# Optimization experiments

Measured on AMD Instinct MI355X. Metric: run time of the kernel, lower is better.

Reference implementation:

```python
import jax, jax.numpy as jnp
import numpy as np

B, S, D, H = 4, 2048, 512, 512

def setup_inputs() -> dict:
    key = jax.random.key(0)
    ks = jax.random.split(key, 9)
    sc_d = 1.0 / np.sqrt(D)
    sc_s = 1.0 / np.sqrt(S)
    return {
        "x": jax.random.normal(ks[0], (B, S, D), dtype=jnp.float32),
        "Wq": jax.random.normal(ks[1], (D, H), dtype=jnp.float32) * sc_d,
        "bq": jnp.zeros((H,), dtype=jnp.float32),
        "Wk": jax.random.normal(ks[2], (D, H), dtype=jnp.float32) * sc_d,
        "bk": jnp.zeros((H,), dtype=jnp.float32),
        "Wv": jax.random.normal(ks[3], (D, H), dtype=jnp.float32) * sc_d,
        "bv": jnp.zeros((H,), dtype=jnp.float32),
        "Wd": jax.random.normal(ks[4], (S, H), dtype=jnp.float32) * sc_s,
        "bd": jnp.zeros((H,), dtype=jnp.float32),
    }

def reference(x, Wq, bq, Wk, bk, Wv, bv, Wd, bd):
    # q, k, v: [B, S, H]
    q = x @ Wq + bq
    k = x @ Wk + bk
    v = x @ Wv + bv
    # raw scores: [B, S, S]
    qk = jnp.einsum('bsh,bth->bst', q, k)
    # Dense+sigmoid over the last (seqlen) axis: [B, S, H]
    dense_out = jax.nn.sigmoid(qk @ Wd + bd)
    # value weights: [B, S, S]
    vw = jnp.einsum('bsh,bth->bst', dense_out, v)
    # out: [B, S, D]
    return jnp.einsum('bst,btd->bsd', vw, x)
```

## Files before the change

kernel.cpp:

```cpp
#include <hip/hip_runtime.h>
#include <hip/hip_bf16.h>
#include <stdint.h>

#define BB 4
#define SS 2048
#define DD 512
#define HH 512

typedef __attribute__((ext_vector_type(8))) short short8;
typedef __attribute__((ext_vector_type(4))) float floatx4;

typedef __attribute__((address_space(3))) uint32_t lds_u32_t;
typedef const __attribute__((address_space(1))) uint32_t glb_u32_t;

__device__ __forceinline__ void gload_lds16(const void* g, void* l) {
  __builtin_amdgcn_global_load_lds((glb_u32_t*)g, (lds_u32_t*)l, 16, 0, 0);
}

__device__ __forceinline__ short f2bf(float f) {
  __hip_bfloat16 h = __float2bfloat16(f);
  return __builtin_bit_cast(short, h);
}

__device__ __forceinline__ float bf2f(short s) {
  uint32_t u = ((uint32_t)(uint16_t)s) << 16;
  return __builtin_bit_cast(float, u);
}

template <int BM>
__device__ __forceinline__ void gemm_mainloop(const short* __restrict__ Ab,
                                              const short* __restrict__ Bb,
                                              int lda, int ldb, int K,
                                              floatx4 (&acc)[BM / 32][4]) {
  constexpr int BK = 64;
  constexpr int MF = BM / 32;
  __shared__ short As[BM * BK];
  __shared__ short Bs[128 * BK];

  const int t = threadIdx.x;
  const int lane = t & 63;
  const int wid = t >> 6;
  const int wr = wid >> 1, wc = wid & 1;
  const int r16 = lane & 15;
  const int hi = lane >> 4;

  const int srow = t >> 3;
  const int schunk = t & 7;

#pragma unroll
  for (int i = 0; i < MF; i++)
#pragma unroll
    for (int j = 0; j < 4; j++) acc[i][j] = (floatx4)0.f;

  for (int k0 = 0; k0 < K; k0 += BK) {
#pragma unroll
    for (int s = 0; s < BM / 32; s++) {
      const int row = s * 32 + srow;
      const int g = schunk ^ (row & 7);
      gload_lds16(Ab + (long)row * lda + k0 + g * 8,
                  &As[row * BK + schunk * 8]);
    }
#pragma unroll
    for (int s = 0; s < 4; s++) {
      const int row = s * 32 + srow;
      const int g = schunk ^ (row & 7);
      gload_lds16(Bb + (long)row * ldb + k0 + g * 8,
                  &Bs[row * BK + schunk * 8]);
    }
    __syncthreads();

    short8 af[MF][2], bfr[4][2];
#pragma unroll
    for (int i = 0; i < MF; i++) {
      const int row = wr * (BM / 2) + i * 16 + r16;
      const int x7 = row & 7;
      af[i][0] = *(const short8*)&As[row * BK + (hi ^ x7) * 8];
      af[i][1] = *(const short8*)&As[row * BK + ((hi + 4) ^ x7) * 8];
    }
#pragma unroll
    for (int j = 0; j < 4; j++) {
      const int row = wc * 64 + j * 16 + r16;
      const int x7 = row & 7;
      bfr[j][0] = *(const short8*)&Bs[row * BK + (hi ^ x7) * 8];
      bfr[j][1] = *(const short8*)&Bs[row * BK + ((hi + 4) ^ x7) * 8];
    }
#pragma unroll
    for (int i = 0; i < MF; i++)
#pragma unroll
      for (int j = 0; j < 4; j++) {
        acc[i][j] = __builtin_amdgcn_mfma_f32_16x16x32_bf16(
            af[i][0], bfr[j][0], acc[i][j], 0, 0, 0);
        acc[i][j] = __builtin_amdgcn_mfma_f32_16x16x32_bf16(
            af[i][1], bfr[j][1], acc[i][j], 0, 0, 0);
      }
    __syncthreads();
  }
}

template <int BM, int EPI>
__device__ __forceinline__ void epilogue_std(floatx4 (&acc)[BM / 32][4],
                                             void* __restrict__ Cm, long c_base,
                                             const float* __restrict__ bias,
                                             int ldc, long row0, long col0) {
  const int lane = threadIdx.x & 63;
  const int wid = threadIdx.x >> 6;
  const int wr = wid >> 1, wc = wid & 1;
  const int r16 = lane & 15;
#pragma unroll
  for (int i = 0; i < BM / 32; i++) {
    const long rbase = row0 + wr * (BM / 2) + i * 16 + (lane >> 4) * 4;
#pragma unroll
    for (int j = 0; j < 4; j++) {
      const long col = col0 + wc * 64 + j * 16 + r16;
      float bv = 0.f;
      if (EPI == 2) bv = bias[col];
#pragma unroll
      for (int rg = 0; rg < 4; rg++) {
        float v = acc[i][j][rg];
        if (EPI == 2) v = 1.f / (1.f + __expf(-(v + bv)));
        const long idx = c_base + (rbase + rg) * ldc + col;
        if (EPI == 3)
          ((float*)Cm)[idx] = v;
        else
          ((__hip_bfloat16*)Cm)[idx] = __float2bfloat16(v);
      }
    }
  }
}

template <int BM, int EPI>
__global__ __launch_bounds__(256) void gemm_bt(
    const short* __restrict__ A, const short* __restrict__ Bm,
    void* __restrict__ Cm, const float* __restrict__ bias, int K, int lda,
    int ldb, int ldc, long sA, long sB, long sC) {
  const int bz = blockIdx.z;
  floatx4 acc[BM / 32][4];
  const long row0 = (long)blockIdx.x * BM, col0 = (long)blockIdx.y * 128;
  gemm_mainloop<BM>(A + bz * sA + row0 * lda, Bm + bz * sB + col0 * ldb, lda,
                    ldb, K, acc);
  epilogue_std<BM, EPI>(acc, Cm, bz * sC, bias, ldc, row0, col0);
}

__global__ __launch_bounds__(256) void gemm_qkv(
    const short* __restrict__ xb, const short* __restrict__ WT,
    const float* __restrict__ bcat, short* __restrict__ q,
    short* __restrict__ kT, short* __restrict__ vT) {
  floatx4 acc[4][4];
  const long row0 = (long)blockIdx.x * 128;
  const int y = blockIdx.y;
  gemm_mainloop<128>(xb + row0 * DD, WT + (long)y * 128 * DD, DD, DD, DD, acc);

  const int lane = threadIdx.x & 63;
  const int wid = threadIdx.x >> 6;
  const int wr = wid >> 1, wc = wid & 1;
  const int r16 = lane & 15;
  const int hi4 = (lane >> 4) * 4;
  const int mode = y >> 2;
  const int b = (int)(row0 >> 11);
  const int sblk = (int)(row0 & 2047);
  short* tp = (mode == 1) ? kT : vT;
#pragma unroll
  for (int i = 0; i < 4; i++) {
    const int s0 = sblk + wr * 64 + i * 16 + hi4;
#pragma unroll
    for (int j = 0; j < 4; j++) {
      const int colg = y * 128 + wc * 64 + j * 16 + r16;
      const float bv = bcat[colg];
      short o[4];
#pragma unroll
      for (int rg = 0; rg < 4; rg++) o[rg] = f2bf(acc[i][j][rg] + bv);
      if (mode == 0) {
#pragma unroll
        for (int rg = 0; rg < 4; rg++)
          q[((long)b * SS + s0 + rg) * HH + colg] = o[rg];
      } else {
        const int cl = colg - mode * 512;
        *(uint64_t*)&tp[((long)b * HH + cl) * SS + s0] = *(uint64_t*)o;
      }
    }
  }
}

__global__ __launch_bounds__(256) void gemm_dual_split(
    const short* __restrict__ WdT, const short* __restrict__ kT,
    short* __restrict__ partM2, const short* __restrict__ xT,
    const short* __restrict__ vT, short* __restrict__ partM3) {
  const int bz = blockIdx.z;
  const int tb = bz >> 2, sp = bz & 3;
  const int task = tb >> 2, b = tb & 3;
  const short* A = (task ? xT + (long)b * HH * SS : WdT) + sp * 512;
  const short* B = (task ? vT : kT) + (long)b * HH * SS + sp * 512;
  short* C = (task ? partM3 : partM2) + ((long)(tb & 3) * 4 + sp) * HH * HH;
  floatx4 acc[2][4];
  const long row0 = (long)blockIdx.x * 64, col0 = (long)blockIdx.y * 128;
  gemm_mainloop<64>(A + row0 * SS, B + col0 * SS, SS, SS, 512, acc);
  epilogue_std<64, 0>(acc, C, 0, nullptr, HH, row0, col0);
}

__global__ __launch_bounds__(256) void reduce_part(
    const short* __restrict__ partM2, const short* __restrict__ partM3,
    short* __restrict__ M2, short* __restrict__ M3t) {
  const int z = blockIdx.z;
  const int b = z & 3;
  const short* src = (z < 4 ? partM2 : partM3) + (long)b * 4 * HH * HH;
  short* dst = (z < 4 ? M2 : M3t) + (long)b * HH * HH;
  const long i = ((long)blockIdx.x * 256 + threadIdx.x) * 8;
  float s[8];
#pragma unroll
  for (int j = 0; j < 8; j++) s[j] = 0.f;
#pragma unroll
  for (int sp = 0; sp < 4; sp++) {
    short8 v = *(const short8*)&src[(long)sp * HH * HH + i];
#pragma unroll
    for (int j = 0; j < 8; j++) s[j] += bf2f(v[j]);
  }
  short o[8];
#pragma unroll
  for (int j = 0; j < 8; j++) o[j] = f2bf(s[j]);
  *(short8*)&dst[i] = *(short8*)o;
}

__global__ void prep(const float* __restrict__ x, const float* __restrict__ Wq,
                     const float* __restrict__ Wk, const float* __restrict__ Wv,
                     const float* __restrict__ Wd, const float* __restrict__ bq,
                     const float* __restrict__ bk, const float* __restrict__ bv,
                     short* __restrict__ xb, short* __restrict__ xT,
                     short* __restrict__ WT, short* __restrict__ WdT,
                     float* __restrict__ bcat) {
  __shared__ float tile[32][33];
  const int z = blockIdx.z, yb = blockIdx.y;
  const int tx = threadIdx.x, ty = threadIdx.y;
  if (z < 4) {
    const long b = z;
    const float* in = x + b * SS * DD;
    const int c0 = blockIdx.x * 32, r0 = yb * 32;
#pragma unroll
    for (int i = 0; i < 32; i += 8) {
      float v = in[(long)(r0 + ty + i) * DD + c0 + tx];
      tile[ty + i][tx] = v;
      xb[(b * SS + r0 + ty + i) * DD + c0 + tx] = f2bf(v);
    }
    __syncthreads();
#pragma unroll
    for (int i = 0; i < 32; i += 8)
      xT[(b * DD + c0 + ty + i) * SS + r0 + tx] = f2bf(tile[tx][ty + i]);
  } else if (z < 7) {
    const int w = z - 4;
    if (yb < 16) {
      const float* in = w == 0 ? Wq : (w == 1 ? Wk : Wv);
      short* out = WT + (long)w * HH * DD;
      const int c0 = blockIdx.x * 32, r0 = yb * 32;
#pragma unroll
      for (int i = 0; i < 32; i += 8)
        tile[ty + i][tx] = in[(long)(r0 + ty + i) * HH + c0 + tx];
      __syncthreads();
#pragma unroll
      for (int i = 0; i < 32; i += 8)
        out[(long)(c0 + ty + i) * DD + r0 + tx] = f2bf(tile[tx][ty + i]);
    } else if (w == 0 && yb < 22 && blockIdx.x == 0) {
      const int i = (yb - 16) * 256 + ty * 32 + tx;
      bcat[i] = i < 512 ? bq[i] : (i < 1024 ? bk[i - 512] : bv[i - 1024]);
    }
  } else {
    const int c0 = blockIdx.x * 32, r0 = yb * 32;
#pragma unroll
    for (int i = 0; i < 32; i += 8)
      tile[ty + i][tx] = Wd[(long)(r0 + ty + i) * HH + c0 + tx];
    __syncthreads();
#pragma unroll
    for (int i = 0; i < 32; i += 8)
      WdT[(long)(c0 + ty + i) * SS + r0 + tx] = f2bf(tile[tx][ty + i]);
  }
}

extern "C" void kernel_launch(void* const* d_in, const int* in_sizes, int n_in,
                              void* d_out, int out_size, void* d_ws,
                              size_t ws_size, hipStream_t stream) {
  (void)in_sizes;
  (void)n_in;
  (void)out_size;
  (void)ws_size;
  const float* x = (const float*)d_in[0];
  const float* Wq = (const float*)d_in[1];
  const float* bq = (const float*)d_in[2];
  const float* Wk = (const float*)d_in[3];
  const float* bk = (const float*)d_in[4];
  const float* Wv = (const float*)d_in[5];
  const float* bv = (const float*)d_in[6];
  const float* Wd = (const float*)d_in[7];
  const float* bd = (const float*)d_in[8];

  char* w = (char*)d_ws;
  auto alloc = [&](size_t bytes) {
    char* p = w;
    w += (bytes + 255) & ~(size_t)255;
    return p;
  };
  short* xb = (short*)alloc((size_t)BB * SS * DD * 2);
  short* xT = (short*)alloc((size_t)BB * DD * SS * 2);
  short* WT = (short*)alloc((size_t)3 * HH * DD * 2);
  short* WdT = (short*)alloc((size_t)HH * SS * 2);
  float* bcat = (float*)alloc((size_t)3 * HH * 4);
  short* q = (short*)alloc((size_t)BB * SS * HH * 2);
  short* kT = (short*)alloc((size_t)BB * HH * SS * 2);
  short* vT = (short*)alloc((size_t)BB * HH * SS * 2);
  short* partM2 = (short*)alloc((size_t)BB * 4 * HH * HH * 2);
  short* partM3 = (short*)alloc((size_t)BB * 4 * HH * HH * 2);
  short* M2 = (short*)alloc((size_t)BB * HH * HH * 2);
  short* M3t = (short*)alloc((size_t)BB * DD * HH * 2);
  short* dense = (short*)alloc((size_t)BB * SS * HH * 2);

  dim3 tb(32, 8);
  prep<<<dim3(16, 64, 8), tb, 0, stream>>>(x, Wq, Wk, Wv, Wd, bq, bk, bv, xb,
                                           xT, WT, WdT, bcat);

  gemm_qkv<<<dim3(BB * SS / 128, 12, 1), 256, 0, stream>>>(xb, WT, bcat, q, kT,
                                                           vT);
  gemm_dual_split<<<dim3(8, 4, 32), 256, 0, stream>>>(WdT, kT, partM2, xT, vT,
                                                      partM3);
  reduce_part<<<dim3(128, 1, 8), 256, 0, stream>>>(partM2, partM3, M2, M3t);
  gemm_bt<64, 2><<<dim3(SS / 64, HH / 128, BB), 256, 0, stream>>>(
      q, M2, dense, bd, HH, HH, HH, HH, (long)SS * HH, (long)HH * HH,
      (long)SS * HH);
  gemm_bt<64, 3><<<dim3(SS / 64, DD / 128, BB), 256, 0, stream>>>(
      dense, M3t, d_out, nullptr, HH, HH, HH, DD, (long)SS * HH, (long)DD * HH,
      (long)SS * DD);
}
```

Before: 81.87 us.

## Fuse dense-sigmoid GEMM and output GEMM into one kernel via LDS

```diff
diff --git a/kernel.cpp b/kernel.cpp
--- a/kernel.cpp
+++ b/kernel.cpp
@@ -97,11 +97,11 @@
   }
 }
 
-template <int BM, int EPI>
-__device__ __forceinline__ void epilogue_std(floatx4 (&acc)[BM / 32][4],
-                                             void* __restrict__ Cm, long c_base,
-                                             const float* __restrict__ bias,
-                                             int ldc, long row0, long col0) {
+template <int BM>
+__device__ __forceinline__ void epilogue_bf16(floatx4 (&acc)[BM / 32][4],
+                                              short* __restrict__ Cm,
+                                              long c_base, int ldc, long row0,
+                                              long col0) {
   const int lane = threadIdx.x & 63;
   const int wid = threadIdx.x >> 6;
   const int wr = wid >> 1, wc = wid & 1;
@@ -112,33 +112,11 @@
 #pragma unroll
     for (int j = 0; j < 4; j++) {
       const long col = col0 + wc * 64 + j * 16 + r16;
-      float bv = 0.f;
-      if (EPI == 2) bv = bias[col];
-#pragma unroll
-      for (int rg = 0; rg < 4; rg++) {
-        float v = acc[i][j][rg];
-        if (EPI == 2) v = 1.f / (1.f + __expf(-(v + bv)));
-        const long idx = c_base + (rbase + rg) * ldc + col;
-        if (EPI == 3)
-          ((float*)Cm)[idx] = v;
-        else
-          ((__hip_bfloat16*)Cm)[idx] = __float2bfloat16(v);
-      }
-    }
-  }
-}
-
-template <int BM, int EPI>
-__global__ __launch_bounds__(256) void gemm_bt(
-    const short* __restrict__ A, const short* __restrict__ Bm,
-    void* __restrict__ Cm, const float* __restrict__ bias, int K, int lda,
-    int ldb, int ldc, long sA, long sB, long sC) {
-  const int bz = blockIdx.z;
-  floatx4 acc[BM / 32][4];
-  const long row0 = (long)blockIdx.x * BM, col0 = (long)blockIdx.y * 128;
-  gemm_mainloop<BM>(A + bz * sA + row0 * lda, Bm + bz * sB + col0 * ldb, lda,
-                    ldb, K, acc);
-  epilogue_std<BM, EPI>(acc, Cm, bz * sC, bias, ldc, row0, col0);
+#pragma unroll
+      for (int rg = 0; rg < 4; rg++)
+        Cm[c_base + (rbase + rg) * ldc + col] = f2bf(acc[i][j][rg]);
+    }
+  }
 }
 
 __global__ __launch_bounds__(256) void gemm_qkv(
@@ -194,7 +172,7 @@
   floatx4 acc[2][4];
   const long row0 = (long)blockIdx.x * 64, col0 = (long)blockIdx.y * 128;
   gemm_mainloop<64>(A + row0 * SS, B + col0 * SS, SS, SS, 512, acc);
-  epilogue_std<64, 0>(acc, C, 0, nullptr, HH, row0, col0);
+  epilogue_bf16<64>(acc, C, 0, HH, row0, col0);
 }
 
 __global__ __launch_bounds__(256) void reduce_part(
@@ -218,6 +196,142 @@
 #pragma unroll
   for (int j = 0; j < 8; j++) o[j] = f2bf(s[j]);
   *(short8*)&dst[i] = *(short8*)o;
+}
+
+__global__ __launch_bounds__(512) void gemm_fused23(
+    const short* __restrict__ q, const short* __restrict__ M2,
+    const short* __restrict__ M3t, const float* __restrict__ bd,
+    float* __restrict__ out) {
+  __shared__ short As[32 * 64];
+  __shared__ short Bs[512 * 64];
+  __shared__ short Ds[32 * 512];
+
+  const int b = blockIdx.z;
+  const long row0 = (long)blockIdx.x * 32;
+  const short* qs = q + ((long)b * SS + row0) * HH;
+  const short* B1 = M2 + (long)b * HH * HH;
+  const short* B2 = M3t + (long)b * DD * HH;
+
+  const int t = threadIdx.x;
+  const int lane = t & 63;
+  const int w = t >> 6;
+  const int r16 = lane & 15;
+  const int hi = lane >> 4;
+
+  floatx4 acc[2][4];
+#pragma unroll
+  for (int i = 0; i < 2; i++)
+#pragma unroll
+    for (int j = 0; j < 4; j++) acc[i][j] = (floatx4)0.f;
+
+  for (int k0 = 0; k0 < 512; k0 += 64) {
+    if (t < 256) {
+      const int row = t >> 3, slot = t & 7;
+      const int g = slot ^ (row & 7);
+      gload_lds16(qs + (long)row * HH + k0 + g * 8, &As[row * 64 + slot * 8]);
+    }
+#pragma unroll
+    for (int i = 0; i < 8; i++) {
+      const int c = i * 512 + t;
+      const int row = c >> 3, slot = c & 7;
+      const int g = slot ^ (row & 7);
+      gload_lds16(B1 + (long)row * HH + k0 + g * 8, &Bs[row * 64 + slot * 8]);
+    }
+    __syncthreads();
+    short8 af[2][2], bf[4][2];
+#pragma unroll
+    for (int i = 0; i < 2; i++) {
+      const int row = i * 16 + r16;
+      const int x7 = row & 7;
+      af[i][0] = *(const short8*)&As[row * 64 + (hi ^ x7) * 8];
+      af[i][1] = *(const short8*)&As[row * 64 + ((hi + 4) ^ x7) * 8];
+    }
+#pragma unroll
+    for (int j = 0; j < 4; j++) {
+      const int row = w * 64 + j * 16 + r16;
+      const int x7 = row & 7;
+      bf[j][0] = *(const short8*)&Bs[row * 64 + (hi ^ x7) * 8];
+      bf[j][1] = *(const short8*)&Bs[row * 64 + ((hi + 4) ^ x7) * 8];
+    }
+#pragma unroll
+    for (int i = 0; i < 2; i++)
+#pragma unroll
+      for (int j = 0; j < 4; j++) {
+        acc[i][j] = __builtin_amdgcn_mfma_f32_16x16x32_bf16(af[i][0], bf[j][0],
+                                                            acc[i][j], 0, 0, 0);
+        acc[i][j] = __builtin_amdgcn_mfma_f32_16x16x32_bf16(af[i][1], bf[j][1],
+                                                            acc[i][j], 0, 0, 0);
+      }
+    __syncthreads();
+  }
+
+#pragma unroll
+  for (int i = 0; i < 2; i++)
+#pragma unroll
+    for (int j = 0; j < 4; j++) {
+      const int col = w * 64 + j * 16 + r16;
+      const float bv = bd[col];
+#pragma unroll
+      for (int rg = 0; rg < 4; rg++) {
+        const int row = i * 16 + hi * 4 + rg;
+        const float v = 1.f / (1.f + __expf(-(acc[i][j][rg] + bv)));
+        Ds[row * 512 + (((col >> 3) ^ (row & 7)) << 3) + (col & 7)] = f2bf(v);
+      }
+    }
+#pragma unroll
+  for (int i = 0; i < 2; i++)
+#pragma unroll
+    for (int j = 0; j < 4; j++) acc[i][j] = (floatx4)0.f;
+  __syncthreads();
+
+  for (int k0 = 0; k0 < 512; k0 += 64) {
+#pragma unroll
+    for (int i = 0; i < 8; i++) {
+      const int c = i * 512 + t;
+      const int row = c >> 3, slot = c & 7;
+      const int g = slot ^ (row & 7);
+      gload_lds16(B2 + (long)row * HH + k0 + g * 8, &Bs[row * 64 + slot * 8]);
+    }
+    __syncthreads();
+    short8 af[2][2], bf[4][2];
+    const int kc = k0 >> 3;
+#pragma unroll
+    for (int i = 0; i < 2; i++) {
+      const int row = i * 16 + r16;
+      const int x7 = row & 7;
+      af[i][0] = *(const short8*)&Ds[row * 512 + (kc + (hi ^ x7)) * 8];
+      af[i][1] = *(const short8*)&Ds[row * 512 + (kc + ((hi + 4) ^ x7)) * 8];
+    }
+#pragma unroll
+    for (int j = 0; j < 4; j++) {
+      const int row = w * 64 + j * 16 + r16;
+      const int x7 = row & 7;
+      bf[j][0] = *(const short8*)&Bs[row * 64 + (hi ^ x7) * 8];
+      bf[j][1] = *(const short8*)&Bs[row * 64 + ((hi + 4) ^ x7) * 8];
+    }
+#pragma unroll
+    for (int i = 0; i < 2; i++)
+#pragma unroll
+      for (int j = 0; j < 4; j++) {
+        acc[i][j] = __builtin_amdgcn_mfma_f32_16x16x32_bf16(af[i][0], bf[j][0],
+                                                            acc[i][j], 0, 0, 0);
+        acc[i][j] = __builtin_amdgcn_mfma_f32_16x16x32_bf16(af[i][1], bf[j][1],
+                                                            acc[i][j], 0, 0, 0);
+      }
+    __syncthreads();
+  }
+
+#pragma unroll
+  for (int i = 0; i < 2; i++)
+#pragma unroll
+    for (int j = 0; j < 4; j++) {
+      const int col = w * 64 + j * 16 + r16;
+#pragma unroll
+      for (int rg = 0; rg < 4; rg++) {
+        const long row = row0 + i * 16 + hi * 4 + rg;
+        out[((long)b * SS + row) * DD + col] = acc[i][j][rg];
+      }
+    }
 }
 
 __global__ void prep(const float* __restrict__ x, const float* __restrict__ Wq,
@@ -308,7 +422,6 @@
   short* partM3 = (short*)alloc((size_t)BB * 4 * HH * HH * 2);
   short* M2 = (short*)alloc((size_t)BB * HH * HH * 2);
   short* M3t = (short*)alloc((size_t)BB * DD * HH * 2);
-  short* dense = (short*)alloc((size_t)BB * SS * HH * 2);
 
   dim3 tb(32, 8);
   prep<<<dim3(16, 64, 8), tb, 0, stream>>>(x, Wq, Wk, Wv, Wd, bq, bk, bv, xb,
@@ -319,10 +432,6 @@
   gemm_dual_split<<<dim3(8, 4, 32), 256, 0, stream>>>(WdT, kT, partM2, xT, vT,
                                                       partM3);
   reduce_part<<<dim3(128, 1, 8), 256, 0, stream>>>(partM2, partM3, M2, M3t);
-  gemm_bt<64, 2><<<dim3(SS / 64, HH / 128, BB), 256, 0, stream>>>(
-      q, M2, dense, bd, HH, HH, HH, HH, (long)SS * HH, (long)HH * HH,
-      (long)SS * HH);
-  gemm_bt<64, 3><<<dim3(SS / 64, DD / 128, BB), 256, 0, stream>>>(
-      dense, M3t, d_out, nullptr, HH, HH, HH, DD, (long)SS * HH, (long)DD * HH,
-      (long)SS * DD);
-}
+  gemm_fused23<<<dim3(SS / 32, 1, BB), 512, 0, stream>>>(q, M2, M3t, bd,
+                                                         (float*)d_out);
+}
```

Measured after the change: 84.92 us. 1.04x slower.

## Reassociate attention products to skip the QKV projection GEMM

Applied to the files above, without the earlier changes.

```diff
diff --git a/kernel.cpp b/kernel.cpp
--- a/kernel.cpp
+++ b/kernel.cpp
@@ -97,11 +97,11 @@
   }
 }
 
-template <int BM, int EPI>
-__device__ __forceinline__ void epilogue_std(floatx4 (&acc)[BM / 32][4],
-                                             void* __restrict__ Cm, long c_base,
-                                             const float* __restrict__ bias,
-                                             int ldc, long row0, long col0) {
+template <int BM>
+__device__ __forceinline__ void epilogue_bf16(floatx4 (&acc)[BM / 32][4],
+                                              short* __restrict__ Cm,
+                                              long c_base, int ldc, long row0,
+                                              long col0) {
   const int lane = threadIdx.x & 63;
   const int wid = threadIdx.x >> 6;
   const int wr = wid >> 1, wc = wid & 1;
@@ -112,13 +112,40 @@
 #pragma unroll
     for (int j = 0; j < 4; j++) {
       const long col = col0 + wc * 64 + j * 16 + r16;
+#pragma unroll
+      for (int rg = 0; rg < 4; rg++)
+        Cm[c_base + (rbase + rg) * ldc + col] = f2bf(acc[i][j][rg]);
+    }
+  }
+}
+
+template <int BM, int EPI>
+__global__ __launch_bounds__(256) void gemm_bt(
+    const short* __restrict__ A, const short* __restrict__ Bm,
+    void* __restrict__ Cm, const float* __restrict__ bias, long sBias, int K,
+    int lda, int ldb, int ldc, long sA, long sB, long sC) {
+  const int bz = blockIdx.z;
+  floatx4 acc[BM / 32][4];
+  const long row0 = (long)blockIdx.x * BM, col0 = (long)blockIdx.y * 128;
+  gemm_mainloop<BM>(A + bz * sA + row0 * lda, Bm + bz * sB + col0 * ldb, lda,
+                    ldb, K, acc);
+  const int lane = threadIdx.x & 63;
+  const int wid = threadIdx.x >> 6;
+  const int wr = wid >> 1, wc = wid & 1;
+  const int r16 = lane & 15;
+#pragma unroll
+  for (int i = 0; i < BM / 32; i++) {
+    const long rbase = row0 + wr * (BM / 2) + i * 16 + (lane >> 4) * 4;
+#pragma unroll
+    for (int j = 0; j < 4; j++) {
+      const long col = col0 + wc * 64 + j * 16 + r16;
       float bv = 0.f;
-      if (EPI == 2) bv = bias[col];
+      if (EPI == 2) bv = bias[bz * sBias + col];
 #pragma unroll
       for (int rg = 0; rg < 4; rg++) {
         float v = acc[i][j][rg];
         if (EPI == 2) v = 1.f / (1.f + __expf(-(v + bv)));
-        const long idx = c_base + (rbase + rg) * ldc + col;
+        const long idx = bz * sC + (rbase + rg) * ldc + col;
         if (EPI == 3)
           ((float*)Cm)[idx] = v;
         else
@@ -128,127 +155,172 @@
   }
 }
 
-template <int BM, int EPI>
-__global__ __launch_bounds__(256) void gemm_bt(
-    const short* __restrict__ A, const short* __restrict__ Bm,
-    void* __restrict__ Cm, const float* __restrict__ bias, int K, int lda,
-    int ldb, int ldc, long sA, long sB, long sC) {
+__global__ __launch_bounds__(256) void gemm_dual_split(
+    const short* __restrict__ WdT, const short* __restrict__ xT,
+    short* __restrict__ partU, short* __restrict__ partG) {
   const int bz = blockIdx.z;
-  floatx4 acc[BM / 32][4];
-  const long row0 = (long)blockIdx.x * BM, col0 = (long)blockIdx.y * 128;
-  gemm_mainloop<BM>(A + bz * sA + row0 * lda, Bm + bz * sB + col0 * ldb, lda,
-                    ldb, K, acc);
-  epilogue_std<BM, EPI>(acc, Cm, bz * sC, bias, ldc, row0, col0);
-}
-
-__global__ __launch_bounds__(256) void gemm_qkv(
-    const short* __restrict__ xb, const short* __restrict__ WT,
-    const float* __restrict__ bcat, short* __restrict__ q,
-    short* __restrict__ kT, short* __restrict__ vT) {
-  floatx4 acc[4][4];
-  const long row0 = (long)blockIdx.x * 128;
-  const int y = blockIdx.y;
-  gemm_mainloop<128>(xb + row0 * DD, WT + (long)y * 128 * DD, DD, DD, DD, acc);
-
+  const int tb = bz >> 2, sp = bz & 3;
+  const int task = tb >> 2, b = tb & 3;
+  const short* xTb = xT + (long)b * DD * SS;
+  const short* A = (task ? xTb : WdT) + sp * 512;
+  const short* B = xTb + sp * 512;
+  short* C = (task ? partG : partU) + ((long)(tb & 3) * 4 + sp) * HH * HH;
+  floatx4 acc[2][4];
+  const long row0 = (long)blockIdx.x * 64, col0 = (long)blockIdx.y * 128;
+  gemm_mainloop<64>(A + row0 * SS, B + col0 * SS, SS, SS, 512, acc);
+  epilogue_bf16<64>(acc, C, 0, HH, row0, col0);
+}
+
+__global__ __launch_bounds__(256) void reduce_part(
+    const short* __restrict__ partU, const short* __restrict__ partG,
+    short* __restrict__ U, short* __restrict__ G,
+    const float* __restrict__ cpart, const float* __restrict__ sxpart,
+    float* __restrict__ c_d, float* __restrict__ s_x) {
+  const int z = blockIdx.z;
+  const int t = threadIdx.x;
+  if (z == 8) {
+    if (blockIdx.x >= 2) return;
+    const int n = blockIdx.x * 256 + t;
+    float s = 0.f;
+    for (int j = 0; j < 64; j++) s += cpart[j * 512 + n];
+    c_d[n] = s;
+    return;
+  }
+  if (z == 9) {
+    if (blockIdx.x >= 8) return;
+    const int idx = blockIdx.x * 256 + t;
+    const int b = idx >> 9, d = idx & 511;
+    float s = 0.f;
+    for (int j = 0; j < 64; j++) s += sxpart[((long)b * 64 + j) * 512 + d];
+    s_x[idx] = s;
+    return;
+  }
+  const int b = z & 3;
+  const short* src = (z < 4 ? partU : partG) + (long)b * 4 * HH * HH;
+  short* dst = (z < 4 ? U : G) + (long)b * HH * HH;
+  const long i = ((long)blockIdx.x * 256 + t) * 8;
+  float s[8];
+#pragma unroll
+  for (int j = 0; j < 8; j++) s[j] = 0.f;
+#pragma unroll
+  for (int sp = 0; sp < 4; sp++) {
+    short8 v = *(const short8*)&src[(long)sp * HH * HH + i];
+#pragma unroll
+    for (int j = 0; j < 8; j++) s[j] += bf2f(v[j]);
+  }
+  short o[8];
+#pragma unroll
+  for (int j = 0; j < 8; j++) o[j] = f2bf(s[j]);
+  *(short8*)&dst[i] = *(short8*)o;
+}
+
+__global__ __launch_bounds__(256) void gemm_small1(
+    const short* __restrict__ U, const short* __restrict__ G,
+    const short* __restrict__ WTk, const short* __restrict__ WTv,
+    const float* __restrict__ c_d, const float* __restrict__ s_x,
+    const float* __restrict__ bk, const float* __restrict__ bv,
+    short* __restrict__ M2, short* __restrict__ M3t) {
+  const int z = blockIdx.z;
+  const int task = z >> 2, b = z & 3;
+  const short* A = (task ? G : U) + (long)b * HH * HH;
+  const short* B = task ? WTv : WTk;
+  short* C = (task ? M3t : M2) + (long)b * HH * HH;
+  const float* rvec = task ? (s_x + b * HH) : c_d;
+  const float* cvec = task ? bv : bk;
+  floatx4 acc[2][4];
+  const long row0 = (long)blockIdx.x * 64, col0 = (long)blockIdx.y * 128;
+  gemm_mainloop<64>(A + row0 * HH, B + col0 * HH, HH, HH, HH, acc);
   const int lane = threadIdx.x & 63;
   const int wid = threadIdx.x >> 6;
   const int wr = wid >> 1, wc = wid & 1;
   const int r16 = lane & 15;
-  const int hi4 = (lane >> 4) * 4;
-  const int mode = y >> 2;
-  const int b = (int)(row0 >> 11);
-  const int sblk = (int)(row0 & 2047);
-  short* tp = (mode == 1) ? kT : vT;
-#pragma unroll
-  for (int i = 0; i < 4; i++) {
-    const int s0 = sblk + wr * 64 + i * 16 + hi4;
+#pragma unroll
+  for (int i = 0; i < 2; i++) {
+    const long rbase = row0 + wr * 32 + i * 16 + (lane >> 4) * 4;
 #pragma unroll
     for (int j = 0; j < 4; j++) {
-      const int colg = y * 128 + wc * 64 + j * 16 + r16;
-      const float bv = bcat[colg];
-      short o[4];
-#pragma unroll
-      for (int rg = 0; rg < 4; rg++) o[rg] = f2bf(acc[i][j][rg] + bv);
-      if (mode == 0) {
-#pragma unroll
-        for (int rg = 0; rg < 4; rg++)
-          q[((long)b * SS + s0 + rg) * HH + colg] = o[rg];
-      } else {
-        const int cl = colg - mode * 512;
-        *(uint64_t*)&tp[((long)b * HH + cl) * SS + s0] = *(uint64_t*)o;
+      const long col = col0 + wc * 64 + j * 16 + r16;
+      const float cb = cvec[col];
+#pragma unroll
+      for (int rg = 0; rg < 4; rg++)
+        C[(rbase + rg) * HH + col] =
+            f2bf(acc[i][j][rg] + rvec[rbase + rg] * cb);
+    }
+  }
+}
+
+__global__ __launch_bounds__(256) void gemm_small2(
+    const short* __restrict__ M2, const short* __restrict__ Wqb,
+    const float* __restrict__ bq, const float* __restrict__ bd,
+    short* __restrict__ W2bT, float* __restrict__ bias2) {
+  const int b = blockIdx.z;
+  if (blockIdx.y == 4) {
+    if (blockIdx.x != 0) return;
+    const short* m = M2 + (long)b * HH * HH;
+    for (int n = threadIdx.x; n < HH; n += 256) {
+      float s = 0.f;
+      for (int h = 0; h < HH; h += 8) {
+        short8 v = *(const short8*)&m[(long)n * HH + h];
+#pragma unroll
+        for (int j = 0; j < 8; j++) s += bq[h + j] * bf2f(v[j]);
       }
-    }
-  }
-}
-
-__global__ __launch_bounds__(256) void gemm_dual_split(
-    const short* __restrict__ WdT, const short* __restrict__ kT,
-    short* __restrict__ partM2, const short* __restrict__ xT,
-    const short* __restrict__ vT, short* __restrict__ partM3) {
-  const int bz = blockIdx.z;
-  const int tb = bz >> 2, sp = bz & 3;
-  const int task = tb >> 2, b = tb & 3;
-  const short* A = (task ? xT + (long)b * HH * SS : WdT) + sp * 512;
-  const short* B = (task ? vT : kT) + (long)b * HH * SS + sp * 512;
-  short* C = (task ? partM3 : partM2) + ((long)(tb & 3) * 4 + sp) * HH * HH;
+      bias2[b * HH + n] = bd[n] + s;
+    }
+    return;
+  }
   floatx4 acc[2][4];
   const long row0 = (long)blockIdx.x * 64, col0 = (long)blockIdx.y * 128;
-  gemm_mainloop<64>(A + row0 * SS, B + col0 * SS, SS, SS, 512, acc);
-  epilogue_std<64, 0>(acc, C, 0, nullptr, HH, row0, col0);
-}
-
-__global__ __launch_bounds__(256) void reduce_part(
-    const short* __restrict__ partM2, const short* __restrict__ partM3,
-    short* __restrict__ M2, short* __restrict__ M3t) {
-  const int z = blockIdx.z;
-  const int b = z & 3;
-  const short* src = (z < 4 ? partM2 : partM3) + (long)b * 4 * HH * HH;
-  short* dst = (z < 4 ? M2 : M3t) + (long)b * HH * HH;
-  const long i = ((long)blockIdx.x * 256 + threadIdx.x) * 8;
-  float s[8];
-#pragma unroll
-  for (int j = 0; j < 8; j++) s[j] = 0.f;
-#pragma unroll
-  for (int sp = 0; sp < 4; sp++) {
-    short8 v = *(const short8*)&src[(long)sp * HH * HH + i];
-#pragma unroll
-    for (int j = 0; j < 8; j++) s[j] += bf2f(v[j]);
-  }
-  short o[8];
-#pragma unroll
-  for (int j = 0; j < 8; j++) o[j] = f2bf(s[j]);
-  *(short8*)&dst[i] = *(short8*)o;
+  gemm_mainloop<64>(M2 + (long)b * HH * HH + row0 * HH, Wqb + col0 * HH, HH,
+                    HH, HH, acc);
+  epilogue_bf16<64>(acc, W2bT + (long)b * HH * HH, 0, HH, row0, col0);
 }
 
 __global__ void prep(const float* __restrict__ x, const float* __restrict__ Wq,
                      const float* __restrict__ Wk, const float* __restrict__ Wv,
-                     const float* __restrict__ Wd, const float* __restrict__ bq,
-                     const float* __restrict__ bk, const float* __restrict__ bv,
-                     short* __restrict__ xb, short* __restrict__ xT,
-                     short* __restrict__ WT, short* __restrict__ WdT,
-                     float* __restrict__ bcat) {
+                     const float* __restrict__ Wd, short* __restrict__ xb,
+                     short* __restrict__ xT, short* __restrict__ Wqb,
+                     short* __restrict__ WTk, short* __restrict__ WTv,
+                     short* __restrict__ WdT, float* __restrict__ cpart,
+                     float* __restrict__ sxpart) {
   __shared__ float tile[32][33];
+  __shared__ float colp[8][32];
   const int z = blockIdx.z, yb = blockIdx.y;
   const int tx = threadIdx.x, ty = threadIdx.y;
   if (z < 4) {
     const long b = z;
     const float* in = x + b * SS * DD;
     const int c0 = blockIdx.x * 32, r0 = yb * 32;
+    float psum = 0.f;
 #pragma unroll
     for (int i = 0; i < 32; i += 8) {
       float v = in[(long)(r0 + ty + i) * DD + c0 + tx];
       tile[ty + i][tx] = v;
+      psum += v;
       xb[(b * SS + r0 + ty + i) * DD + c0 + tx] = f2bf(v);
     }
+    colp[ty][tx] = psum;
     __syncthreads();
 #pragma unroll
     for (int i = 0; i < 32; i += 8)
       xT[(b * DD + c0 + ty + i) * SS + r0 + tx] = f2bf(tile[tx][ty + i]);
+    if (ty == 0) {
+      float s = 0.f;
+#pragma unroll
+      for (int j = 0; j < 8; j++) s += colp[j][tx];
+      sxpart[(b * 64 + yb) * 512 + c0 + tx] = s;
+    }
+  } else if (z == 4) {
+    if (yb < 16) {
+      const int c0 = blockIdx.x * 32, r0 = yb * 32;
+#pragma unroll
+      for (int i = 0; i < 32; i += 8)
+        Wqb[(long)(r0 + ty + i) * HH + c0 + tx] =
+            f2bf(Wq[(long)(r0 + ty + i) * HH + c0 + tx]);
+    }
   } else if (z < 7) {
-    const int w = z - 4;
     if (yb < 16) {
-      const float* in = w == 0 ? Wq : (w == 1 ? Wk : Wv);
-      short* out = WT + (long)w * HH * DD;
+      const float* in = (z == 5) ? Wk : Wv;
+      short* out = (z == 5) ? WTk : WTv;
       const int c0 = blockIdx.x * 32, r0 = yb * 32;
 #pragma unroll
       for (int i = 0; i < 32; i += 8)
@@ -257,19 +329,27 @@
 #pragma unroll
       for (int i = 0; i < 32; i += 8)
         out[(long)(c0 + ty + i) * DD + r0 + tx] = f2bf(tile[tx][ty + i]);
-    } else if (w == 0 && yb < 22 && blockIdx.x == 0) {
-      const int i = (yb - 16) * 256 + ty * 32 + tx;
-      bcat[i] = i < 512 ? bq[i] : (i < 1024 ? bk[i - 512] : bv[i - 1024]);
     }
   } else {
     const int c0 = blockIdx.x * 32, r0 = yb * 32;
-#pragma unroll
-    for (int i = 0; i < 32; i += 8)
-      tile[ty + i][tx] = Wd[(long)(r0 + ty + i) * HH + c0 + tx];
+    float psum = 0.f;
+#pragma unroll
+    for (int i = 0; i < 32; i += 8) {
+      float v = Wd[(long)(r0 + ty + i) * HH + c0 + tx];
+      tile[ty + i][tx] = v;
+      psum += v;
+    }
+    colp[ty][tx] = psum;
     __syncthreads();
 #pragma unroll
     for (int i = 0; i < 32; i += 8)
       WdT[(long)(c0 + ty + i) * SS + r0 + tx] = f2bf(tile[tx][ty + i]);
+    if (ty == 0) {
+      float s = 0.f;
+#pragma unroll
+      for (int j = 0; j < 8; j++) s += colp[j][tx];
+      cpart[yb * 512 + c0 + tx] = s;
+    }
   }
 }
 
@@ -298,31 +378,38 @@
   };
   short* xb = (short*)alloc((size_t)BB * SS * DD * 2);
   short* xT = (short*)alloc((size_t)BB * DD * SS * 2);
-  short* WT = (short*)alloc((size_t)3 * HH * DD * 2);
+  short* Wqb = (short*)alloc((size_t)DD * HH * 2);
+  short* WTk = (short*)alloc((size_t)HH * DD * 2);
+  short* WTv = (short*)alloc((size_t)HH * DD * 2);
   short* WdT = (short*)alloc((size_t)HH * SS * 2);
-  float* bcat = (float*)alloc((size_t)3 * HH * 4);
-  short* q = (short*)alloc((size_t)BB * SS * HH * 2);
-  short* kT = (short*)alloc((size_t)BB * HH * SS * 2);
-  short* vT = (short*)alloc((size_t)BB * HH * SS * 2);
-  short* partM2 = (short*)alloc((size_t)BB * 4 * HH * HH * 2);
-  short* partM3 = (short*)alloc((size_t)BB * 4 * HH * HH * 2);
+  float* cpart = (float*)alloc((size_t)64 * 512 * 4);
+  float* sxpart = (float*)alloc((size_t)BB * 64 * 512 * 4);
+  float* c_d = (float*)alloc((size_t)512 * 4);
+  float* s_x = (float*)alloc((size_t)BB * 512 * 4);
+  float* bias2 = (float*)alloc((size_t)BB * 512 * 4);
+  short* partU = (short*)alloc((size_t)BB * 4 * HH * HH * 2);
+  short* partG = (short*)alloc((size_t)BB * 4 * HH * HH * 2);
+  short* U = (short*)alloc((size_t)BB * HH * HH * 2);
+  short* G = (short*)alloc((size_t)BB * HH * HH * 2);
   short* M2 = (short*)alloc((size_t)BB * HH * HH * 2);
   short* M3t = (short*)alloc((size_t)BB * DD * HH * 2);
+  short* W2bT = (short*)alloc((size_t)BB * HH * DD * 2);
   short* dense = (short*)alloc((size_t)BB * SS * HH * 2);
 
   dim3 tb(32, 8);
-  prep<<<dim3(16, 64, 8), tb, 0, stream>>>(x, Wq, Wk, Wv, Wd, bq, bk, bv, xb,
-                                           xT, WT, WdT, bcat);
-
-  gemm_qkv<<<dim3(BB * SS / 128, 12, 1), 256, 0, stream>>>(xb, WT, bcat, q, kT,
-                                                           vT);
-  gemm_dual_split<<<dim3(8, 4, 32), 256, 0, stream>>>(WdT, kT, partM2, xT, vT,
-                                                      partM3);
-  reduce_part<<<dim3(128, 1, 8), 256, 0, stream>>>(partM2, partM3, M2, M3t);
+  prep<<<dim3(16, 64, 8), tb, 0, stream>>>(x, Wq, Wk, Wv, Wd, xb, xT, Wqb, WTk,
+                                           WTv, WdT, cpart, sxpart);
+
+  gemm_dual_split<<<dim3(8, 4, 32), 256, 0, stream>>>(WdT, xT, partU, partG);
+  reduce_part<<<dim3(128, 1, 10), 256, 0, stream>>>(partU, partG, U, G, cpart,
+                                                    sxpart, c_d, s_x);
+  gemm_small1<<<dim3(8, 4, 8), 256, 0, stream>>>(U, G, WTk, WTv, c_d, s_x, bk,
+                                                 bv, M2, M3t);
+  gemm_small2<<<dim3(8, 5, 4), 256, 0, stream>>>(M2, Wqb, bq, bd, W2bT, bias2);
   gemm_bt<64, 2><<<dim3(SS / 64, HH / 128, BB), 256, 0, stream>>>(
-      q, M2, dense, bd, HH, HH, HH, HH, (long)SS * HH, (long)HH * HH,
-      (long)SS * HH);
+      xb, W2bT, dense, bias2, HH, DD, DD, DD, HH, (long)SS * DD,
+      (long)HH * DD, (long)SS * HH);
   gemm_bt<64, 3><<<dim3(SS / 64, DD / 128, BB), 256, 0, stream>>>(
-      dense, M3t, d_out, nullptr, HH, HH, HH, DD, (long)SS * HH, (long)DD * HH,
-      (long)SS * DD);
-}
+      dense, M3t, d_out, nullptr, 0, HH, HH, HH, DD, (long)SS * HH,
+      (long)DD * HH, (long)SS * DD);
+}
```

New measurement: 90.66 us. 10.7% more time.

## Fuse split-K partial reduction into dual GEMM via last-block atomic counter

Applied to the files above, without the earlier changes.

```diff
diff --git a/kernel.cpp b/kernel.cpp
--- a/kernel.cpp
+++ b/kernel.cpp
@@ -184,40 +184,57 @@
 __global__ __launch_bounds__(256) void gemm_dual_split(
     const short* __restrict__ WdT, const short* __restrict__ kT,
     short* __restrict__ partM2, const short* __restrict__ xT,
-    const short* __restrict__ vT, short* __restrict__ partM3) {
+    const short* __restrict__ vT, short* __restrict__ partM3,
+    int* __restrict__ cnt, short* __restrict__ M2, short* __restrict__ M3t) {
   const int bz = blockIdx.z;
   const int tb = bz >> 2, sp = bz & 3;
   const int task = tb >> 2, b = tb & 3;
   const short* A = (task ? xT + (long)b * HH * SS : WdT) + sp * 512;
   const short* B = (task ? vT : kT) + (long)b * HH * SS + sp * 512;
-  short* C = (task ? partM3 : partM2) + ((long)(tb & 3) * 4 + sp) * HH * HH;
+  short* parts = task ? partM3 : partM2;
+  short* C = parts + ((long)b * 4 + sp) * HH * HH;
   floatx4 acc[2][4];
   const long row0 = (long)blockIdx.x * 64, col0 = (long)blockIdx.y * 128;
   gemm_mainloop<64>(A + row0 * SS, B + col0 * SS, SS, SS, 512, acc);
   epilogue_std<64, 0>(acc, C, 0, nullptr, HH, row0, col0);
-}
-
-__global__ __launch_bounds__(256) void reduce_part(
-    const short* __restrict__ partM2, const short* __restrict__ partM3,
-    short* __restrict__ M2, short* __restrict__ M3t) {
-  const int z = blockIdx.z;
-  const int b = z & 3;
-  const short* src = (z < 4 ? partM2 : partM3) + (long)b * 4 * HH * HH;
-  short* dst = (z < 4 ? M2 : M3t) + (long)b * HH * HH;
-  const long i = ((long)blockIdx.x * 256 + threadIdx.x) * 8;
-  float s[8];
-#pragma unroll
-  for (int j = 0; j < 8; j++) s[j] = 0.f;
-#pragma unroll
-  for (int sp = 0; sp < 4; sp++) {
-    short8 v = *(const short8*)&src[(long)sp * HH * HH + i];
-#pragma unroll
-    for (int j = 0; j < 8; j++) s[j] += bf2f(v[j]);
-  }
-  short o[8];
-#pragma unroll
-  for (int j = 0; j < 8; j++) o[j] = f2bf(s[j]);
-  *(short8*)&dst[i] = *(short8*)o;
+
+  const int t = threadIdx.x;
+  const int tileid = (tb * 8 + blockIdx.x) * 4 + blockIdx.y;
+  __shared__ int is_last;
+  __threadfence();
+  __syncthreads();
+  if (t == 0) is_last = (atomicAdd(&cnt[tileid], 1) == 3);
+  __syncthreads();
+  if (!is_last) return;
+  __threadfence();
+
+  short* dst = (task ? M3t : M2) + (long)b * HH * HH;
+  const long row = row0 + (t >> 2);
+  const long c0 = col0 + (long)(t & 3) * 32;
+#pragma unroll
+  for (int ch = 0; ch < 4; ch++) {
+    float s[8];
+#pragma unroll
+    for (int j = 0; j < 8; j++) s[j] = 0.f;
+#pragma unroll
+    for (int sp2 = 0; sp2 < 4; sp2++) {
+      const unsigned long long* p =
+          (const unsigned long long*)&parts[((long)b * 4 + sp2) * HH * HH +
+                                            row * HH + c0 + ch * 8];
+      unsigned long long lo =
+          __hip_atomic_load(p, __ATOMIC_RELAXED, __HIP_MEMORY_SCOPE_AGENT);
+      unsigned long long hi =
+          __hip_atomic_load(p + 1, __ATOMIC_RELAXED, __HIP_MEMORY_SCOPE_AGENT);
+#pragma unroll
+      for (int j = 0; j < 4; j++) s[j] += bf2f((short)(lo >> (16 * j)));
+#pragma unroll
+      for (int j = 0; j < 4; j++) s[4 + j] += bf2f((short)(hi >> (16 * j)));
+    }
+    short o[8];
+#pragma unroll
+    for (int j = 0; j < 8; j++) o[j] = f2bf(s[j]);
+    *(short8*)&dst[row * HH + c0 + ch * 8] = *(short8*)o;
+  }
 }
 
 __global__ void prep(const float* __restrict__ x, const float* __restrict__ Wq,
@@ -226,7 +243,7 @@
                      const float* __restrict__ bk, const float* __restrict__ bv,
                      short* __restrict__ xb, short* __restrict__ xT,
                      short* __restrict__ WT, short* __restrict__ WdT,
-                     float* __restrict__ bcat) {
+                     float* __restrict__ bcat, int* __restrict__ cnt) {
   __shared__ float tile[32][33];
   const int z = blockIdx.z, yb = blockIdx.y;
   const int tx = threadIdx.x, ty = threadIdx.y;
@@ -262,6 +279,7 @@
       bcat[i] = i < 512 ? bq[i] : (i < 1024 ? bk[i - 512] : bv[i - 1024]);
     }
   } else {
+    if (yb == 0 && blockIdx.x == 0) cnt[ty * 32 + tx] = 0;
     const int c0 = blockIdx.x * 32, r0 = yb * 32;
 #pragma unroll
     for (int i = 0; i < 32; i += 8)
@@ -301,6 +319,7 @@
   short* WT = (short*)alloc((size_t)3 * HH * DD * 2);
   short* WdT = (short*)alloc((size_t)HH * SS * 2);
   float* bcat = (float*)alloc((size_t)3 * HH * 4);
+  int* cnt = (int*)alloc((size_t)256 * 4);
   short* q = (short*)alloc((size_t)BB * SS * HH * 2);
   short* kT = (short*)alloc((size_t)BB * HH * SS * 2);
   short* vT = (short*)alloc((size_t)BB * HH * SS * 2);
@@ -312,13 +331,12 @@
 
   dim3 tb(32, 8);
   prep<<<dim3(16, 64, 8), tb, 0, stream>>>(x, Wq, Wk, Wv, Wd, bq, bk, bv, xb,
-                                           xT, WT, WdT, bcat);
+                                           xT, WT, WdT, bcat, cnt);
 
   gemm_qkv<<<dim3(BB * SS / 128, 12, 1), 256, 0, stream>>>(xb, WT, bcat, q, kT,
                                                            vT);
   gemm_dual_split<<<dim3(8, 4, 32), 256, 0, stream>>>(WdT, kT, partM2, xT, vT,
-                                                      partM3);
-  reduce_part<<<dim3(128, 1, 8), 256, 0, stream>>>(partM2, partM3, M2, M3t);
+                                                      partM3, cnt, M2, M3t);
   gemm_bt<64, 2><<<dim3(SS / 64, HH / 128, BB), 256, 0, stream>>>(
       q, M2, dense, bd, HH, HH, HH, HH, (long)SS * HH, (long)HH * HH,
       (long)SS * HH);
```

Result: slower. 272.1 us (+232.4%).
